# Kernel optimization log

Hardware: AMD Instinct MI355X
Metric: run time of the kernel (lower is better)

The kernel has to match this reference:

```python
import jax, jax.numpy as jnp
import numpy as np

H, DH = 16, 64  # heads, dim_head (inner_dim = 1024)


def _sdpa(q, k, v):
    # q: (B, Q, D), k/v: (B, K, D); scale = 1/sqrt(D) as in F.scaled_dot_product_attention
    scale = 1.0 / jnp.sqrt(jnp.asarray(q.shape[-1], q.dtype))
    s = jnp.einsum('bqd,bkd->bqk', q, k) * scale
    return jnp.einsum('bqk,bkd->bqd', jax.nn.softmax(s, axis=-1), v)


def setup_inputs() -> dict:
    key = jax.random.key(0)
    ks = jax.random.split(key, 3)
    b, f, n, dim = 8, 16, 196, 1024
    N = 1 + f * n  # CLS + frames*patches = 3137
    x = jax.random.normal(ks[0], (b, N, dim), jnp.float32)
    w_qkv = jax.random.normal(ks[1], (3 * H * DH, dim), jnp.float32) * 0.02
    w_out = jax.random.normal(ks[2], (dim, H * DH), jnp.float32) * 0.02
    b_out = jnp.zeros((dim,), jnp.float32)
    return {"x": x, "w_qkv": w_qkv, "w_out": w_out, "b_out": b_out, "f": f}


def reference(x, w_qkv, w_out, b_out, f):
    b, N, dim = x.shape
    n = (N - 1) // f  # patches per frame

    qkv = x @ w_qkv.T  # (b, N, 3*H*DH)
    q, k, v = jnp.split(qkv, 3, axis=-1)

    def to_bh(t):  # 'b n (h d) -> (b h) n d'
        return t.reshape(b, N, H, DH).transpose(0, 2, 1, 3).reshape(b * H, N, DH)

    q, k, v = map(to_bh, (q, k, v))

    cls_q, q_ = q[:, :1], q[:, 1:]
    cls_k, k_ = k[:, :1], k[:, 1:]
    cls_v, v_ = v[:, :1], v[:, 1:]

    # CLS token attends over all tokens
    cls_out = _sdpa(cls_q, k, v)  # (b*H, 1, DH)

    # spatial attention: '(b h) (f n) d -> (b h f) n d'
    def to_space(t):
        return t.reshape(b * H, f, n, DH).reshape(b * H * f, n, DH)

    q_, k_, v_ = map(to_space, (q_, k_, v_))

    # repeat_interleave CLS k/v over the f groups, then prepend
    ck = jnp.repeat(cls_k, f, axis=0)  # (b*H*f, 1, DH)
    cv = jnp.repeat(cls_v, f, axis=0)
    k_ = jnp.concatenate((ck, k_), axis=1)  # (b*H*f, n+1, DH)
    v_ = jnp.concatenate((cv, v_), axis=1)

    out = _sdpa(q_, k_, v_)  # (b*H*f, n, DH)
    out = out.reshape(b * H, f * n, DH)  # '(b f) n d -> b (f n) d'
    out = jnp.concatenate((cls_out, out), axis=1)  # (b*H, N, DH)
    # '(b h) n d -> b n (h d)'
    out = out.reshape(b, H, N, DH).transpose(0, 2, 1, 3).reshape(b, N, H * DH)
    return out @ w_out.T + b_out
```

## Files before the change

kernel.cpp:

```cpp
#include <hip/hip_runtime.h>
#include <cstdint>
#include <cstddef>

#define DEVINL __device__ __forceinline__

typedef __attribute__((ext_vector_type(8))) short short8;
typedef __attribute__((ext_vector_type(4))) float f32x4;
typedef unsigned short u16;
typedef unsigned int u32;

DEVINL u16 f2b(float f) {
    u32 u = __float_as_uint(f);
    u32 r = (u + 0x7fffu + ((u >> 16) & 1u)) >> 16;
    return (u16)r;
}
DEVINL float b2f(u16 h) { return __uint_as_float(((u32)h) << 16); }

DEVINL void gl_lds16(const void* g, void* l) {
    __builtin_amdgcn_global_load_lds(
        (const __attribute__((address_space(1))) void*)g,
        (__attribute__((address_space(3))) void*)l, 16, 0, 0);
}

#define MROWS   25096
#define NTOK    3137
#define QE      25698304
#define LOG2E   1.4426950408889634f
#define SCL2    0.1803368801111204f

__global__ __launch_bounds__(256) void cvt_kernel(const float* __restrict__ in,
                                                  u16* __restrict__ out, int n4) {
    int i = blockIdx.x * blockDim.x + threadIdx.x;
    int stride = gridDim.x * blockDim.x;
    for (int j = i; j < n4; j += stride) {
        float4 v = ((const float4*)in)[j];
        ushort4 o;
        o.x = f2b(v.x); o.y = f2b(v.y); o.z = f2b(v.z); o.w = f2b(v.w);
        ((ushort4*)out)[j] = o;
    }
}


#define LDS_BUF 32768
#define NTILES  16

template <int MODE>
__global__ __launch_bounds__(512, 2) void gemm256(const u16* __restrict__ A,
                                                  const u16* __restrict__ B,
                                                  u16* __restrict__ q_out,
                                                  u16* __restrict__ k_out,
                                                  u16* __restrict__ v_out,
                                                  const float* __restrict__ bias,
                                                  float* __restrict__ f_out, int M) {
    __shared__ u16 lds[2 * LDS_BUF];
    const int tid = threadIdx.x, lane = tid & 63, w = tid >> 6;
    const int Mm1 = M - 1;

    const u32 nwg = gridDim.x * gridDim.y;
    const u32 orig = blockIdx.y * gridDim.x + blockIdx.x;
    const u32 q8 = nwg >> 3, r8 = nwg & 7, xcd = orig & 7, rest = orig >> 3;
    const u32 wg = (xcd < r8 ? xcd * (q8 + 1) : r8 * (q8 + 1) + (xcd - r8) * q8) + rest;
    const int m0 = (int)(wg / gridDim.x) * 256;
    const int n0 = (int)(wg % gridDim.x) * 256;

    const int wm = w >> 2, wn = w & 3;

    const int stRow = lane >> 2;
    const int stCol = (((lane & 3) ^ ((lane >> 3) & 3)) << 3);

    const int slotOff = (((lane >> 4) ^ ((lane >> 1) & 3)) << 3);
    const int rdA = (wm * 128 + (lane & 15)) * 32 + slotOff;
    const int rdB = (wn * 64 + (lane & 15)) * 32 + slotOff + 16384;

#define STAGE_A(NB, KK, KT) do {                                              \
    _Pragma("unroll") for (int j_ = 0; j_ < 2; ++j_) {                        \
        const int c_ = (w << 1) | j_;                                         \
        int r_ = m0 + c_ * 16 + stRow; if (r_ > Mm1) r_ = Mm1;                \
        gl_lds16(A + (size_t)r_ * 1024 + (KT) + (KK) * 32 + stCol,            \
                 lds + (NB) + (KK) * 8192 + c_ * 512);                        \
    } } while (0)

#define STAGE_B(NB, KK, KT) do {                                              \
    _Pragma("unroll") for (int j_ = 0; j_ < 2; ++j_) {                        \
        const int c_ = (w << 1) | j_;                                         \
        const int r_ = n0 + c_ * 16 + stRow;                                  \
        gl_lds16(B + (size_t)r_ * 1024 + (KT) + (KK) * 32 + stCol,            \
                 lds + (NB) + 16384 + (KK) * 8192 + c_ * 512);                \
    } } while (0)

#define LDA4(CB, KK, MB) do {                                                 \
    _Pragma("unroll") for (int i_ = 0; i_ < 4; ++i_)                          \
        aF[i_] = *(const short8*)&lds[(CB) + (KK) * 8192 + rdA +              \
                                      ((MB) + i_) * 16 * 32];                 \
    } while (0)

#define LDB4(CB, KK) do {                                                     \
    _Pragma("unroll") for (int i_ = 0; i_ < 4; ++i_)                          \
        bF[i_] = *(const short8*)&lds[(CB) + (KK) * 8192 + rdB +              \
                                      i_ * 16 * 32];                          \
    } while (0)

#define MFMA16(MB) do {                                                       \
    _Pragma("unroll") for (int i_ = 0; i_ < 4; ++i_)                          \
        _Pragma("unroll") for (int n_ = 0; n_ < 4; ++n_)                      \
            acc[(MB) + i_][n_] = __builtin_amdgcn_mfma_f32_16x16x32_bf16(     \
                aF[i_], bF[n_], acc[(MB) + i_][n_], 0, 0, 0);                 \
    } while (0)

#define LGKM0_FENCE() do {                                                    \
    asm volatile("s_waitcnt lgkmcnt(0)" ::: "memory");                        \
    __builtin_amdgcn_sched_barrier(0); } while (0)

    f32x4 acc[8][4];
    const f32x4 zf = {0.f, 0.f, 0.f, 0.f};
#pragma unroll
    for (int i = 0; i < 8; ++i)
#pragma unroll
        for (int j = 0; j < 4; ++j) acc[i][j] = zf;

    STAGE_A(0, 0, 0);
    STAGE_B(0, 0, 0);
    STAGE_A(0, 1, 0);
    STAGE_B(0, 1, 0);
    asm volatile("s_waitcnt vmcnt(4)" ::: "memory");
    __builtin_amdgcn_sched_barrier(0);
    __builtin_amdgcn_s_barrier();

    for (int T = 0; T < NTILES; ++T) {
        const int cb = (T & 1) * LDS_BUF;
        const int nb = ((T + 1) & 1) * LDS_BUF;
        const bool pf = (T < NTILES - 1);
        const int kt1 = (T + 1) * 64;

        short8 aF[4], bF[4];

        LDA4(cb, 0, 0);
        LDB4(cb, 0);
        if (pf) { STAGE_A(nb, 0, kt1); STAGE_B(nb, 0, kt1); }
        __builtin_amdgcn_s_barrier();
        LGKM0_FENCE();
        __builtin_amdgcn_s_setprio(1);
        MFMA16(0);
        __builtin_amdgcn_s_setprio(0);
        __builtin_amdgcn_s_barrier();

        LDA4(cb, 0, 4);
        if (pf) { STAGE_A(nb, 1, kt1); STAGE_B(nb, 1, kt1); }
        __builtin_amdgcn_s_barrier();
        LGKM0_FENCE();
        __builtin_amdgcn_s_setprio(1);
        MFMA16(4);
        __builtin_amdgcn_s_setprio(0);
        if (pf) { asm volatile("s_waitcnt vmcnt(8)" ::: "memory"); }
        else    { asm volatile("s_waitcnt vmcnt(0)" ::: "memory"); }
        __builtin_amdgcn_sched_barrier(0);
        __builtin_amdgcn_s_barrier();

        LDA4(cb, 1, 0);
        LDB4(cb, 1);
        __builtin_amdgcn_s_barrier();
        LGKM0_FENCE();
        __builtin_amdgcn_s_setprio(1);
        MFMA16(0);
        __builtin_amdgcn_s_setprio(0);
        __builtin_amdgcn_s_barrier();

        LDA4(cb, 1, 4);
        __builtin_amdgcn_s_barrier();
        LGKM0_FENCE();
        __builtin_amdgcn_s_setprio(1);
        MFMA16(4);
        __builtin_amdgcn_s_setprio(0);
        if (pf) {
            asm volatile("s_waitcnt vmcnt(4)" ::: "memory");
            __builtin_amdgcn_sched_barrier(0);
        }
        __builtin_amdgcn_s_barrier();
    }

#pragma unroll
    for (int m = 0; m < 8; ++m) {
#pragma unroll
        for (int n = 0; n < 4; ++n) {
#pragma unroll
            for (int r = 0; r < 4; ++r) {
                const int gm = m0 + wm * 128 + m * 16 + ((lane >> 4) << 2) + r;
                if (gm < M) {
                    const int gc = n0 + wn * 64 + n * 16 + (lane & 15);
                    if (MODE == 0) {
                        const int t = gc >> 10;
                        const int h = (gc >> 6) & 15;
                        const int d = gc & 63;
                        const u32 bb = (u32)gm / 3137u;
                        const u32 nn = (u32)gm - bb * 3137u;
                        u16* dst = (t == 0) ? q_out : (t == 1) ? k_out : v_out;
                        dst[(((size_t)(bb * 16 + h)) * NTOK + nn) * 64 + d] =
                            f2b(acc[m][n][r]);
                    } else {
                        f_out[(size_t)gm * 1024 + gc] = acc[m][n][r] + bias[gc];
                    }
                }
            }
        }
    }
#undef STAGE_A
#undef STAGE_B
#undef LDA4
#undef LDB4
#undef MFMA16
#undef LGKM0_FENCE
}

#define CSZ 393
__global__ __launch_bounds__(256) void attn_cls_part(const u16* __restrict__ qb,
                                                     const u16* __restrict__ kb,
                                                     const u16* __restrict__ vb,
                                                     float* __restrict__ part) {
    const int bid = blockIdx.x;
    const int bh = bid >> 3, c = bid & 7;
    const size_t base = (size_t)bh * NTOK * 64;
    const int tid = threadIdx.x, lane = tid & 63, wid = tid >> 6;
    const int j0 = c * CSZ;
    const int cnt = min(NTOK - j0, CSZ);

    __shared__ float qs[64];
    __shared__ float sc[CSZ];
    __shared__ float redbuf[8];
    __shared__ float ored[4][64];

    if (tid < 64) qs[tid] = b2f(qb[base + tid]);
    __syncthreads();

    for (int j = tid; j < cnt; j += 256) {
        const u16* kr = kb + base + (size_t)(j0 + j) * 64;
        float acc = 0.f;
#pragma unroll
        for (int c2 = 0; c2 < 8; ++c2) {
            short8 v8 = *(const short8*)(kr + c2 * 8);
#pragma unroll
            for (int t = 0; t < 8; ++t) acc += qs[c2 * 8 + t] * b2f((u16)v8[t]);
        }
        sc[j] = acc * 0.125f;
    }
    __syncthreads();

    float mx = -1e30f;
    for (int j = tid; j < cnt; j += 256) mx = fmaxf(mx, sc[j]);
#pragma unroll
    for (int m = 32; m >= 1; m >>= 1) mx = fmaxf(mx, __shfl_xor(mx, m));
    if (lane == 0) redbuf[wid] = mx;
    __syncthreads();
    mx = fmaxf(fmaxf(redbuf[0], redbuf[1]), fmaxf(redbuf[2], redbuf[3]));

    float sum = 0.f;
    for (int j = tid; j < cnt; j += 256) {
        float p = exp2f((sc[j] - mx) * LOG2E);
        sc[j] = p;
        sum += p;
    }
#pragma unroll
    for (int m = 32; m >= 1; m >>= 1) sum += __shfl_xor(sum, m);
    if (lane == 0) redbuf[4 + wid] = sum;
    __syncthreads();
    const float tot = redbuf[4] + redbuf[5] + redbuf[6] + redbuf[7];

    const int d = tid & 63, g = tid >> 6;
    float o = 0.f;
    for (int j = g; j < cnt; j += 4)
        o += sc[j] * b2f(vb[base + (size_t)(j0 + j) * 64 + d]);
    ored[g][d] = o;
    __syncthreads();

    float* pb = part + (size_t)bid * 66;
    if (tid < 64) pb[2 + tid] = ored[0][tid] + ored[1][tid] + ored[2][tid] + ored[3][tid];
    else if (tid == 64) pb[0] = mx;
    else if (tid == 65) pb[1] = tot;
}

__global__ __launch_bounds__(64) void attn_cls_fin(const float* __restrict__ part,
                                                   u16* __restrict__ attnb) {
    const int bh = blockIdx.x, d = threadIdx.x;
    const int bb = bh >> 4, h = bh & 15;
    float m = -1e30f;
#pragma unroll
    for (int c = 0; c < 8; ++c) m = fmaxf(m, part[(size_t)(bh * 8 + c) * 66]);
    float t = 0.f, o = 0.f;
#pragma unroll
    for (int c = 0; c < 8; ++c) {
        const float* pb = part + (size_t)(bh * 8 + c) * 66;
        const float w = exp2f((pb[0] - m) * LOG2E);
        t += w * pb[1];
        o += w * pb[2 + d];
    }
    attnb[(size_t)bb * NTOK * 1024 + h * 64 + d] = f2b(o / t);
}

__global__ __launch_bounds__(256) void attn_spatial(const u16* __restrict__ qb,
                                                    const u16* __restrict__ kb,
                                                    const u16* __restrict__ vb,
                                                    u16* __restrict__ attnb) {
    const int blk = blockIdx.x;
    const int bh = blk >> 4, fi = blk & 15;
    const int bb = bh >> 4, h = bh & 15;
    const int tid = threadIdx.x, lane = tid & 63, wid = tid >> 6;
    const int hi = lane >> 4, lo = lane & 15;
    const size_t kvbase = (size_t)bh * NTOK * 64;

    __shared__ u16 Kl[208 * 68];
    __shared__ u16 Vt[64 * 208];
    __shared__ u16 Pl[4 * 16 * 208];

    u16* Ptmp = Pl;
    const short8 z8 = {0, 0, 0, 0, 0, 0, 0, 0};
    for (int idx = tid; idx < 208 * 8; idx += 256) {
        const int j = idx >> 3, c = idx & 7;
        short8 kval = z8;
        if (j < 197) {
            const int n = (j == 0) ? 0 : (1 + fi * 196 + (j - 1));
            kval = *(const short8*)(kb + kvbase + (size_t)n * 64 + c * 8);
            *(short8*)(Ptmp + ((j * 64 + c * 8) ^ ((j & 7) << 3))) =
                *(const short8*)(vb + kvbase + (size_t)n * 64 + c * 8);
        }
        *(short8*)(Kl + j * 68 + c * 8) = kval;
    }
    __syncthreads();
#pragma unroll
    for (int c = 0; c < 8; ++c) {
        if (tid < 197) {
            short8 v8 = *(const short8*)(Ptmp + ((tid * 64 + c * 8) ^ ((tid & 7) << 3)));
#pragma unroll
            for (int t = 0; t < 8; ++t) Vt[(c * 8 + t) * 208 + tid] = (u16)v8[t];
        }
    }
    for (int idx = tid; idx < 64 * 11; idx += 256)
        Vt[(idx / 11) * 208 + 197 + (idx % 11)] = 0;
    __syncthreads();

    u16* pl = Pl + wid * 16 * 208;
    const f32x4 zf = {0.f, 0.f, 0.f, 0.f};

    for (int mf = wid; mf < 13; mf += 4) {
        int qr = mf * 16 + lo; if (qr > 195) qr = 195;
        const u16* qp = qb + kvbase + (size_t)(1 + fi * 196 + qr) * 64 + hi * 8;
        const short8 a0 = *(const short8*)(qp);
        const short8 a1 = *(const short8*)(qp + 32);

        f32x4 s[13];
#pragma unroll
        for (int nf = 0; nf < 13; ++nf) s[nf] = zf;
#pragma unroll
        for (int nf = 0; nf < 13; ++nf) {
            const u16* kp = Kl + (nf * 16 + lo) * 68 + hi * 8;
            const short8 b0 = *(const short8*)(kp);
            const short8 b1 = *(const short8*)(kp + 32);
            s[nf] = __builtin_amdgcn_mfma_f32_16x16x32_bf16(a0, b0, s[nf], 0, 0, 0);
            s[nf] = __builtin_amdgcn_mfma_f32_16x16x32_bf16(a1, b1, s[nf], 0, 0, 0);
        }

        float rls[4];
#pragma unroll
        for (int reg = 0; reg < 4; ++reg) {
            float mx = s[0][reg];
#pragma unroll
            for (int nf = 1; nf < 13; ++nf) mx = fmaxf(mx, s[nf][reg]);
            mx = fmaxf(mx, __shfl_xor(mx, 1));
            mx = fmaxf(mx, __shfl_xor(mx, 2));
            mx = fmaxf(mx, __shfl_xor(mx, 4));
            mx = fmaxf(mx, __shfl_xor(mx, 8));
            const float mC = mx * SCL2;
            float sum = 0.f;
#pragma unroll
            for (int nf = 0; nf < 13; ++nf) {
                const float p = exp2f(fmaf(s[nf][reg], SCL2, -mC));
                s[nf][reg] = p;
                sum += p;
            }
            sum += __shfl_xor(sum, 1);
            sum += __shfl_xor(sum, 2);
            sum += __shfl_xor(sum, 4);
            sum += __shfl_xor(sum, 8);
            rls[reg] = 1.0f / (sum - 11.0f * exp2f(-mC));
        }

#pragma unroll
        for (int nf = 0; nf < 13; ++nf)
#pragma unroll
            for (int reg = 0; reg < 4; ++reg)
                pl[(hi * 4 + reg) * 208 + nf * 16 + lo] = f2b(s[nf][reg]);

        f32x4 o[4];
#pragma unroll
        for (int i = 0; i < 4; ++i) o[i] = zf;
#pragma unroll
        for (int kk = 0; kk < 6; ++kk) {
            const short8 pa = *(const short8*)(pl + lo * 208 + kk * 32 + hi * 8);
#pragma unroll
            for (int nf2 = 0; nf2 < 4; ++nf2) {
                const short8 bvv =
                    *(const short8*)(Vt + (nf2 * 16 + lo) * 208 + kk * 32 + hi * 8);
                o[nf2] = __builtin_amdgcn_mfma_f32_16x16x32_bf16(pa, bvv, o[nf2], 0, 0, 0);
            }
        }
        {
            const u16* pap = pl + lo * 208 + 192 + (hi < 2 ? hi * 8 : 0);
            short8 pa = *(const short8*)pap;
            if (hi >= 2) pa = z8;
#pragma unroll
            for (int nf2 = 0; nf2 < 4; ++nf2) {
                const u16* bvp = Vt + (nf2 * 16 + lo) * 208 + 192 + (hi < 2 ? hi * 8 : 0);
                short8 bvv = *(const short8*)bvp;
                if (hi >= 2) bvv = z8;
                o[nf2] = __builtin_amdgcn_mfma_f32_16x16x32_bf16(pa, bvv, o[nf2], 0, 0, 0);
            }
        }

#pragma unroll
        for (int nf2 = 0; nf2 < 4; ++nf2)
#pragma unroll
            for (int reg = 0; reg < 4; ++reg) {
                const int r = mf * 16 + hi * 4 + reg;
                if (r < 196) {
                    const int d = nf2 * 16 + lo;
                    const size_t nn = 1 + fi * 196 + r;
                    attnb[((size_t)bb * NTOK + nn) * 1024 + h * 64 + d] =
                        f2b(o[nf2][reg] * rls[reg]);
                }
            }
    }
}

extern "C" void kernel_launch(void* const* d_in, const int* in_sizes, int n_in,
                              void* d_out, int out_size, void* d_ws, size_t ws_size,
                              hipStream_t stream) {
    const float* x = (const float*)d_in[0];
    const float* w_qkv = (const float*)d_in[1];
    const float* w_out = (const float*)d_in[2];
    const float* b_out = (const float*)d_in[3];

    const size_t need = ((size_t)QE * 2 + 3145728 + 1048576) * 2;
    if (ws_size < need) {
        hipMemsetAsync(d_out, 0, (size_t)out_size * 4, stream);
        return;
    }

    u16* vb = (u16*)d_ws;
    u16* xab = vb + QE;
    u16* wqb = xab + QE;
    u16* wob = wqb + 3145728;
    u16* qb = (u16*)d_out;
    u16* kb = qb + QE;
    float* outf = (float*)d_out;
    float* clsp = (float*)wqb;

    cvt_kernel<<<2048, 256, 0, stream>>>(x, xab, QE / 4);
    cvt_kernel<<<2048, 256, 0, stream>>>(w_qkv, wqb, 3145728 / 4);
    cvt_kernel<<<1024, 256, 0, stream>>>(w_out, wob, 1048576 / 4);

    gemm256<0><<<dim3(12, 99), 512, 0, stream>>>(xab, wqb, qb, kb, vb, nullptr,
                                                 nullptr, MROWS);
    attn_cls_part<<<1024, 256, 0, stream>>>(qb, kb, vb, clsp);
    attn_cls_fin<<<128, 64, 0, stream>>>(clsp, xab);
    attn_spatial<<<2048, 256, 0, stream>>>(qb, kb, vb, xab);
    gemm256<1><<<dim3(4, 99), 512, 0, stream>>>(xab, wob, nullptr, nullptr, nullptr,
                                                b_out, outf, MROWS);
}
```

Measured before the change: 517.3 us.

## Keep softmax probabilities in registers, swizzle K LDS, restage GEMM prefetch

The spatial attention kernel now computes S^T, with K as the A operand, so each lane holds one query column. This lets the max and sum reductions use two cross-row shuffles. The normalized probabilities are packed to bf16 in registers and passed to the PV MFMA through lane shuffles instead of a per-wave LDS P buffer. K is stored in an XOR-swizzled LDS layout and V is transposed directly during the global load, which removes the staging pass and one sync. With the reduced LDS footprint, the kernel requests 3 blocks per CU. The GEMM spreads the next-tile A/B staging evenly across the four sub-phases, with a matching waitcnt adjustment.

New measurement: 457.2 us. -11.6%, faster.

```diff
diff --git a/kernel.cpp b/kernel.cpp
--- a/kernel.cpp
+++ b/kernel.cpp
@@ -39,7 +39,6 @@
         ((ushort4*)out)[j] = o;
     }
 }
-
 
 #define LDS_BUF 32768
 #define NTILES  16
@@ -136,7 +135,7 @@
 
         LDA4(cb, 0, 0);
         LDB4(cb, 0);
-        if (pf) { STAGE_A(nb, 0, kt1); STAGE_B(nb, 0, kt1); }
+        if (pf) STAGE_A(nb, 0, kt1);
         __builtin_amdgcn_s_barrier();
         LGKM0_FENCE();
         __builtin_amdgcn_s_setprio(1);
@@ -145,19 +144,20 @@
         __builtin_amdgcn_s_barrier();
 
         LDA4(cb, 0, 4);
-        if (pf) { STAGE_A(nb, 1, kt1); STAGE_B(nb, 1, kt1); }
+        if (pf) STAGE_B(nb, 0, kt1);
         __builtin_amdgcn_s_barrier();
         LGKM0_FENCE();
         __builtin_amdgcn_s_setprio(1);
         MFMA16(4);
         __builtin_amdgcn_s_setprio(0);
-        if (pf) { asm volatile("s_waitcnt vmcnt(8)" ::: "memory"); }
+        if (pf) { asm volatile("s_waitcnt vmcnt(4)" ::: "memory"); }
         else    { asm volatile("s_waitcnt vmcnt(0)" ::: "memory"); }
         __builtin_amdgcn_sched_barrier(0);
         __builtin_amdgcn_s_barrier();
 
         LDA4(cb, 1, 0);
         LDB4(cb, 1);
+        if (pf) STAGE_A(nb, 1, kt1);
         __builtin_amdgcn_s_barrier();
         LGKM0_FENCE();
         __builtin_amdgcn_s_setprio(1);
@@ -166,6 +166,7 @@
         __builtin_amdgcn_s_barrier();
 
         LDA4(cb, 1, 4);
+        if (pf) STAGE_B(nb, 1, kt1);
         __builtin_amdgcn_s_barrier();
         LGKM0_FENCE();
         __builtin_amdgcn_s_setprio(1);
@@ -295,10 +296,10 @@
     attnb[(size_t)bb * NTOK * 1024 + h * 64 + d] = f2b(o / t);
 }
 
-__global__ __launch_bounds__(256) void attn_spatial(const u16* __restrict__ qb,
-                                                    const u16* __restrict__ kb,
-                                                    const u16* __restrict__ vb,
-                                                    u16* __restrict__ attnb) {
+__global__ __launch_bounds__(256, 3) void attn_spatial(const u16* __restrict__ qb,
+                                                       const u16* __restrict__ kb,
+                                                       const u16* __restrict__ vb,
+                                                       u16* __restrict__ attnb) {
     const int blk = blockIdx.x;
     const int bh = blk >> 4, fi = blk & 15;
     const int bb = bh >> 4, h = bh & 15;
@@ -306,111 +307,114 @@
     const int hi = lane >> 4, lo = lane & 15;
     const size_t kvbase = (size_t)bh * NTOK * 64;
 
-    __shared__ u16 Kl[208 * 68];
+    __shared__ u16 Kl[208 * 64];
     __shared__ u16 Vt[64 * 208];
-    __shared__ u16 Pl[4 * 16 * 208];
-
-    u16* Ptmp = Pl;
+
     const short8 z8 = {0, 0, 0, 0, 0, 0, 0, 0};
+
     for (int idx = tid; idx < 208 * 8; idx += 256) {
         const int j = idx >> 3, c = idx & 7;
         short8 kval = z8;
         if (j < 197) {
             const int n = (j == 0) ? 0 : (1 + fi * 196 + (j - 1));
             kval = *(const short8*)(kb + kvbase + (size_t)n * 64 + c * 8);
-            *(short8*)(Ptmp + ((j * 64 + c * 8) ^ ((j & 7) << 3))) =
-                *(const short8*)(vb + kvbase + (size_t)n * 64 + c * 8);
-        }
-        *(short8*)(Kl + j * 68 + c * 8) = kval;
-    }
-    __syncthreads();
-#pragma unroll
-    for (int c = 0; c < 8; ++c) {
-        if (tid < 197) {
-            short8 v8 = *(const short8*)(Ptmp + ((tid * 64 + c * 8) ^ ((tid & 7) << 3)));
-#pragma unroll
-            for (int t = 0; t < 8; ++t) Vt[(c * 8 + t) * 208 + tid] = (u16)v8[t];
-        }
-    }
-    for (int idx = tid; idx < 64 * 11; idx += 256)
-        Vt[(idx / 11) * 208 + 197 + (idx % 11)] = 0;
-    __syncthreads();
-
-    u16* pl = Pl + wid * 16 * 208;
+            const short8 v8 = *(const short8*)(vb + kvbase + (size_t)n * 64 + c * 8);
+#pragma unroll
+            for (int t0 = 0; t0 < 8; ++t0) {
+                const int t = (t0 + c) & 7;
+                Vt[(c * 8 + t) * 208 + j] = (u16)v8[t];
+            }
+        } else {
+#pragma unroll
+            for (int t = 0; t < 8; ++t) Vt[(c * 8 + t) * 208 + j] = 0;
+        }
+        *(short8*)(Kl + ((j * 64 + c * 8) ^ ((j & 7) << 3))) = kval;
+    }
+    __syncthreads();
+
+    const int ksw = (lo & 7) << 3;
+    const int src0 = lo + ((hi & 1) << 5);
+    const int src1 = src0 + 16;
     const f32x4 zf = {0.f, 0.f, 0.f, 0.f};
 
     for (int mf = wid; mf < 13; mf += 4) {
         int qr = mf * 16 + lo; if (qr > 195) qr = 195;
         const u16* qp = qb + kvbase + (size_t)(1 + fi * 196 + qr) * 64 + hi * 8;
-        const short8 a0 = *(const short8*)(qp);
-        const short8 a1 = *(const short8*)(qp + 32);
+        const short8 qb0 = *(const short8*)(qp);
+        const short8 qb1 = *(const short8*)(qp + 32);
 
         f32x4 s[13];
 #pragma unroll
         for (int nf = 0; nf < 13; ++nf) s[nf] = zf;
 #pragma unroll
         for (int nf = 0; nf < 13; ++nf) {
-            const u16* kp = Kl + (nf * 16 + lo) * 68 + hi * 8;
-            const short8 b0 = *(const short8*)(kp);
-            const short8 b1 = *(const short8*)(kp + 32);
-            s[nf] = __builtin_amdgcn_mfma_f32_16x16x32_bf16(a0, b0, s[nf], 0, 0, 0);
-            s[nf] = __builtin_amdgcn_mfma_f32_16x16x32_bf16(a1, b1, s[nf], 0, 0, 0);
-        }
-
-        float rls[4];
-#pragma unroll
-        for (int reg = 0; reg < 4; ++reg) {
-            float mx = s[0][reg];
-#pragma unroll
-            for (int nf = 1; nf < 13; ++nf) mx = fmaxf(mx, s[nf][reg]);
-            mx = fmaxf(mx, __shfl_xor(mx, 1));
-            mx = fmaxf(mx, __shfl_xor(mx, 2));
-            mx = fmaxf(mx, __shfl_xor(mx, 4));
-            mx = fmaxf(mx, __shfl_xor(mx, 8));
-            const float mC = mx * SCL2;
-            float sum = 0.f;
-#pragma unroll
-            for (int nf = 0; nf < 13; ++nf) {
+            const int e0 = (nf * 16 + lo) * 64 + hi * 8;
+            const short8 a0 = *(const short8*)(Kl + (e0 ^ ksw));
+            const short8 a1 = *(const short8*)(Kl + ((e0 + 32) ^ ksw));
+            s[nf] = __builtin_amdgcn_mfma_f32_16x16x32_bf16(a0, qb0, s[nf], 0, 0, 0);
+            s[nf] = __builtin_amdgcn_mfma_f32_16x16x32_bf16(a1, qb1, s[nf], 0, 0, 0);
+        }
+
+        float mx = s[0][0];
+#pragma unroll
+        for (int nf = 0; nf < 13; ++nf)
+#pragma unroll
+            for (int reg = 0; reg < 4; ++reg) mx = fmaxf(mx, s[nf][reg]);
+        mx = fmaxf(mx, __shfl_xor(mx, 16));
+        mx = fmaxf(mx, __shfl_xor(mx, 32));
+        const float mC = mx * SCL2;
+        float sum = 0.f;
+#pragma unroll
+        for (int nf = 0; nf < 13; ++nf)
+#pragma unroll
+            for (int reg = 0; reg < 4; ++reg) {
                 const float p = exp2f(fmaf(s[nf][reg], SCL2, -mC));
                 s[nf][reg] = p;
                 sum += p;
             }
-            sum += __shfl_xor(sum, 1);
-            sum += __shfl_xor(sum, 2);
-            sum += __shfl_xor(sum, 4);
-            sum += __shfl_xor(sum, 8);
-            rls[reg] = 1.0f / (sum - 11.0f * exp2f(-mC));
-        }
-
-#pragma unroll
-        for (int nf = 0; nf < 13; ++nf)
-#pragma unroll
-            for (int reg = 0; reg < 4; ++reg)
-                pl[(hi * 4 + reg) * 208 + nf * 16 + lo] = f2b(s[nf][reg]);
+        sum += __shfl_xor(sum, 16);
+        sum += __shfl_xor(sum, 32);
+        const float rls = 1.0f / (sum - 11.0f * exp2f(-mC));
+
+        u32 w0[13], w1[13];
+#pragma unroll
+        for (int nf = 0; nf < 13; ++nf) {
+            const float p0 = s[nf][0] * rls, p1 = s[nf][1] * rls;
+            const float p2 = s[nf][2] * rls, p3 = s[nf][3] * rls;
+            asm("v_cvt_pk_bf16_f32 %0, %1, %2" : "=v"(w0[nf]) : "v"(p0), "v"(p1));
+            asm("v_cvt_pk_bf16_f32 %0, %1, %2" : "=v"(w1[nf]) : "v"(p2), "v"(p3));
+        }
 
         f32x4 o[4];
 #pragma unroll
         for (int i = 0; i < 4; ++i) o[i] = zf;
 #pragma unroll
-        for (int kk = 0; kk < 6; ++kk) {
-            const short8 pa = *(const short8*)(pl + lo * 208 + kk * 32 + hi * 8);
+        for (int kk = 0; kk < 7; ++kk) {
+            u32 x0, x1, x2, x3;
+            if (kk < 6) {
+                const u32 aA0 = __shfl(w0[2 * kk], src0), aA1 = __shfl(w1[2 * kk], src0);
+                const u32 aA2 = __shfl(w0[2 * kk], src1), aA3 = __shfl(w1[2 * kk], src1);
+                const u32 aB0 = __shfl(w0[2 * kk + 1], src0), aB1 = __shfl(w1[2 * kk + 1], src0);
+                const u32 aB2 = __shfl(w0[2 * kk + 1], src1), aB3 = __shfl(w1[2 * kk + 1], src1);
+                const bool lh = hi < 2;
+                x0 = lh ? aA0 : aB0; x1 = lh ? aA1 : aB1;
+                x2 = lh ? aA2 : aB2; x3 = lh ? aA3 : aB3;
+            } else {
+                const u32 aA0 = __shfl(w0[12], src0), aA1 = __shfl(w1[12], src0);
+                const u32 aA2 = __shfl(w0[12], src1), aA3 = __shfl(w1[12], src1);
+                const bool lh = hi < 2;
+                x0 = lh ? aA0 : 0u; x1 = lh ? aA1 : 0u;
+                x2 = lh ? aA2 : 0u; x3 = lh ? aA3 : 0u;
+            }
+            union { u32 u[4]; short8 v; } pu;
+            pu.u[0] = x0; pu.u[1] = x1; pu.u[2] = x2; pu.u[3] = x3;
+            const short8 pa = pu.v;
 #pragma unroll
             for (int nf2 = 0; nf2 < 4; ++nf2) {
-                const short8 bvv =
-                    *(const short8*)(Vt + (nf2 * 16 + lo) * 208 + kk * 32 + hi * 8);
-                o[nf2] = __builtin_amdgcn_mfma_f32_16x16x32_bf16(pa, bvv, o[nf2], 0, 0, 0);
-            }
-        }
-        {
-            const u16* pap = pl + lo * 208 + 192 + (hi < 2 ? hi * 8 : 0);
-            short8 pa = *(const short8*)pap;
-            if (hi >= 2) pa = z8;
-#pragma unroll
-            for (int nf2 = 0; nf2 < 4; ++nf2) {
-                const u16* bvp = Vt + (nf2 * 16 + lo) * 208 + 192 + (hi < 2 ? hi * 8 : 0);
-                short8 bvv = *(const short8*)bvp;
-                if (hi >= 2) bvv = z8;
-                o[nf2] = __builtin_amdgcn_mfma_f32_16x16x32_bf16(pa, bvv, o[nf2], 0, 0, 0);
+                short8 bv = z8;
+                if (kk < 6 || hi < 2)
+                    bv = *(const short8*)(Vt + (nf2 * 16 + lo) * 208 + kk * 32 + hi * 8);
+                o[nf2] = __builtin_amdgcn_mfma_f32_16x16x32_bf16(pa, bv, o[nf2], 0, 0, 0);
             }
         }
 
@@ -423,7 +427,7 @@
                     const int d = nf2 * 16 + lo;
                     const size_t nn = 1 + fi * 196 + r;
                     attnb[((size_t)bb * NTOK + nn) * 1024 + h * 64 + d] =
-                        f2b(o[nf2][reg] * rls[reg]);
+                        f2b(o[nf2][reg]);
                 }
             }
     }
```
